# Performance work log

Measured on AMD Instinct MI355X. Metric: run time of the kernel, lower is better.

Reference implementation:

```python
import jax, jax.numpy as jnp
import numpy as np

N, M, D, O = 1_000_000, 64, 3, 2


def _rbf(A, B, sf, ell):
    # squared-exponential kernel: sf^2 * exp(-||a/ell - b/ell||^2 / 2)
    A = A / ell
    B = B / ell
    sq = (jnp.sum(A * A, axis=1)[:, None]
          + jnp.sum(B * B, axis=1)[None, :]
          - 2.0 * (A @ B.T))
    return (sf * sf) * jnp.exp(-sq / 2.0)


def setup_inputs() -> dict:
    key = jax.random.key(0)
    k1, k2, k3, k4 = jax.random.split(key, 4)
    X = jax.random.uniform(k1, (N, D), dtype=jnp.float32) * 10.0  # query points
    t = jax.random.normal(k2, (N,), dtype=jnp.float32)            # unused by forward (matches torch)
    Z = jax.random.uniform(k3, (M, D), dtype=jnp.float32) * 10.0  # inducing points (well-separated -> Kzz well-conditioned)
    U = jax.random.normal(k4, (M, O), dtype=jnp.float32)          # learned inducing outputs
    return {"t": t, "X": X, "Z": Z, "U": U, "sf": 1.0, "ell": 1.0}


def reference(t, X, Z, U, sf, ell):
    # Precompute (as in __init__): Kzz, its inverse, Cholesky factor, and their product.
    Kzz = _rbf(Z, Z, sf, ell)                      # [M, M]
    L = jnp.linalg.cholesky(Kzz)                   # [M, M]
    KzzinvL = jnp.linalg.inv(Kzz) @ L              # [M, M]
    # Forward: T = K(X, Z) @ KzzinvL ; out = T @ U
    Kxz = _rbf(X, Z, sf, ell)                      # [N, M] -- dominant memory traffic
    return (Kxz @ KzzinvL) @ U                     # [N, O]
```

## Files before the change

kernel.cpp:

```cpp
#include <hip/hip_runtime.h>
#include <hip/hip_bf16.h>
#include <utility>

#define LOG2E 1.4426950408889634f

#if __has_builtin(__builtin_amdgcn_exp2f)
#define EXP2F(x) __builtin_amdgcn_exp2f(x)
#else
#define EXP2F(x) exp2f(x)
#endif

#if __has_builtin(__builtin_amdgcn_rsqf)
#define RSQ(x) __builtin_amdgcn_rsqf(x)
#else
#define RSQ(x) (1.0f / sqrtf(x))
#endif

#define RDLANE(x, l) __int_as_float(__builtin_amdgcn_readlane(__float_as_int(x), (l)))

typedef float f16v __attribute__((ext_vector_type(16)));
struct Rows { f16v v0, v1, v2, v3; };

template<int J> __device__ __forceinline__ float getR(const Rows& r) {
    if constexpr (J < 16)      return r.v0[J];
    else if constexpr (J < 32) return r.v1[J - 16];
    else if constexpr (J < 48) return r.v2[J - 32];
    else                       return r.v3[J - 48];
}
template<int J> __device__ __forceinline__ void setR(Rows& r, float x) {
    if constexpr (J < 16)      r.v0[J] = x;
    else if constexpr (J < 32) r.v1[J - 16] = x;
    else if constexpr (J < 48) r.v2[J - 32] = x;
    else                       r.v3[J - 48] = x;
}

template<int LO, int W>
__device__ __forceinline__ float selR(const Rows& r, int k) {
    if constexpr (W == 1) {
        return getR<LO>(r);
    } else {
        float lo = selR<LO, W / 2>(r, k);
        float hi = selR<LO + W / 2, W / 2>(r, k);
        return (k & (W / 2)) ? hi : lo;
    }
}

template<int Q>
__device__ __forceinline__ void upd_quad(Rows& r, float lk, const float4 lv) {
    setR<4 * Q + 0>(r, fmaf(-lk, lv.x, getR<4 * Q + 0>(r)));
    setR<4 * Q + 1>(r, fmaf(-lk, lv.y, getR<4 * Q + 1>(r)));
    setR<4 * Q + 2>(r, fmaf(-lk, lv.z, getR<4 * Q + 2>(r)));
    setR<4 * Q + 3>(r, fmaf(-lk, lv.w, getR<4 * Q + 3>(r)));
}
template<int QLO, int... Qs>
__device__ __forceinline__ void upd_quads(Rows& r, float lk, const float4* lkb4,
                                          std::integer_sequence<int, Qs...>) {
    (upd_quad<QLO + Qs>(r, lk, lkb4[QLO + Qs]), ...);
}

template<int... Js>
__device__ __forceinline__ void load_row(Rows& r, const float* Lrow,
                                         std::integer_sequence<int, Js...>) {
    (setR<Js>(r, Lrow[Js]), ...);
}

template<int KLO, int KHI, int ULO>
__device__ __forceinline__ void chol_phase(Rows& r, float* Lsh, float* lkbuf,
                                           int lane) {
    const float4* lkb4 = (const float4*)lkbuf;
#pragma clang loop unroll(disable)
    for (int k = KLO; k < KHI; ++k) {
        float rk  = selR<ULO, 64 - ULO>(r, k);
        float dk  = RDLANE(rk, k);
        float inv = RSQ(dk);
        float lk  = rk * inv;
        float st  = (lane == k) ? inv : lk;
        Lsh[lane * 65 + k] = st;
        lkbuf[lane] = lk;
        __syncthreads();
        upd_quads<ULO / 4>(r, lk, lkb4,
                           std::make_integer_sequence<int, 16 - ULO / 4>{});
        __syncthreads();
    }
}

__global__ __launch_bounds__(64, 1)
void gp_precompute(const float* __restrict__ Z, const float* __restrict__ U,
                   const float* __restrict__ sf_p, const float* __restrict__ ell_p,
                   float* __restrict__ ws) {
    __shared__ float Lsh[64 * 65];
    __shared__ float4 zbuf[64];
    __shared__ __align__(16) float lkbuf[64];
    const int lane = threadIdx.x;
    const float sf  = sf_p[0];
    const float ell = ell_p[0];
    const float inv_ell = 1.0f / ell;
    const float sf2 = sf * sf;

    const float z0 = Z[lane * 3 + 0] * inv_ell;
    const float z1 = Z[lane * 3 + 1] * inv_ell;
    const float z2 = Z[lane * 3 + 2] * inv_ell;

    zbuf[lane] = make_float4(z0, z1, z2, 0.0f);
    __syncthreads();

#pragma unroll 4
    for (int j = 0; j < 64; ++j) {
        float4 zj = zbuf[j];
        float dx = z0 - zj.x;
        float dy = z1 - zj.y;
        float dz = z2 - zj.z;
        float sq = dx * dx + dy * dy + dz * dz;
        Lsh[lane * 65 + j] = sf2 * EXP2F(-0.5f * LOG2E * sq);
    }
    __syncthreads();

    Rows r;
    load_row(r, &Lsh[lane * 65], std::make_integer_sequence<int, 64>{});

    chol_phase< 0, 32,  0>(r, Lsh, lkbuf, lane);
    chol_phase<32, 48, 32>(r, Lsh, lkbuf, lane);
    chol_phase<48, 64, 48>(r, Lsh, lkbuf, lane);
    __syncthreads();

    float s0 = U[lane * 2 + 0];
    float s1 = U[lane * 2 + 1];
    float w0v = 0.0f, w1v = 0.0f;
#pragma unroll 8
    for (int i = 63; i >= 0; --i) {
        float a   = Lsh[i * 65 + lane];
        float rdi = RDLANE(a, i);
        float w0  = RDLANE(s0, i) * rdi;
        float w1  = RDLANE(s1, i) * rdi;
        bool  me  = (lane == i);
        w0v = me ? w0 : w0v;
        w1v = me ? w1 : w1v;
        s0 = fmaf(-a, w0, s0);
        s1 = fmaf(-a, w1, s1);
    }

    const float dm = -0.5f * LOG2E * (z0 * z0 + z1 * z1 + z2 * z2);
    float4* ws4 = (float4*)ws;
    ws4[lane * 2 + 0] = make_float4(z0, z1, z2, dm);
    ws4[lane * 2 + 1] = make_float4(sf2 * w0v, sf2 * w1v, 0.0f, 0.0f);
}

__global__ __launch_bounds__(256) void gp_forward(const float* __restrict__ X,
                                                  const float* __restrict__ ws,
                                                  const float* __restrict__ ell_p,
                                                  float* __restrict__ out, int n) {
    __shared__ float4 P[128];
    for (int i = threadIdx.x; i < 128; i += 256)
        P[i] = ((const float4*)ws)[i];
    const float inv_ell = 1.0f / ell_p[0];
    __syncthreads();

    const int t  = blockIdx.x * 256 + threadIdx.x;
    const int i0 = 2 * t;

    float p00, p01, p02, p10, p11, p12;
    if (i0 + 1 < n) {
        const float2* X2 = (const float2*)X;
        float2 xa = X2[3 * t + 0];
        float2 xb = X2[3 * t + 1];
        float2 xc = X2[3 * t + 2];
        p00 = xa.x; p01 = xa.y; p02 = xb.x;
        p10 = xb.y; p11 = xc.x; p12 = xc.y;
    } else if (i0 < n) {
        p00 = X[3 * i0 + 0]; p01 = X[3 * i0 + 1]; p02 = X[3 * i0 + 2];
        p10 = p00; p11 = p01; p12 = p02;
    } else {
        p00 = p01 = p02 = p10 = p11 = p12 = 0.0f;
    }

    float xt0[2], xt1[2], xt2[2], c[2];
    {
        float xs0 = p00 * inv_ell, xs1 = p01 * inv_ell, xs2 = p02 * inv_ell;
        c[0]  = -0.5f * LOG2E * (xs0 * xs0 + xs1 * xs1 + xs2 * xs2);
        xt0[0] = xs0 * LOG2E; xt1[0] = xs1 * LOG2E; xt2[0] = xs2 * LOG2E;
        xs0 = p10 * inv_ell; xs1 = p11 * inv_ell; xs2 = p12 * inv_ell;
        c[1]  = -0.5f * LOG2E * (xs0 * xs0 + xs1 * xs1 + xs2 * xs2);
        xt0[1] = xs0 * LOG2E; xt1[1] = xs1 * LOG2E; xt2[1] = xs2 * LOG2E;
    }

    float acc0[2] = {0.f, 0.f};
    float acc1[2] = {0.f, 0.f};

#pragma unroll 4
    for (int m = 0; m < 64; ++m) {
        const float4 a = P[2 * m + 0];
        const float4 b = P[2 * m + 1];
#pragma unroll
        for (int p = 0; p < 2; ++p) {
            float arg = fmaf(xt0[p], a.x,
                        fmaf(xt1[p], a.y,
                        fmaf(xt2[p], a.z, c[p] + a.w)));
            float e = EXP2F(arg);
            acc0[p] = fmaf(e, b.x, acc0[p]);
            acc1[p] = fmaf(e, b.y, acc1[p]);
        }
    }

    if (i0 + 1 < n) {
        ((float4*)out)[t] = make_float4(acc0[0], acc1[0], acc0[1], acc1[1]);
    } else if (i0 < n) {
        ((float2*)out)[i0] = make_float2(acc0[0], acc1[0]);
    }
}

extern "C" void kernel_launch(void* const* d_in, const int* in_sizes, int n_in,
                              void* d_out, int out_size, void* d_ws, size_t ws_size,
                              hipStream_t stream) {
    const float* X    = (const float*)d_in[1];
    const float* Z    = (const float*)d_in[2];
    const float* U    = (const float*)d_in[3];
    const float* sf   = (const float*)d_in[4];
    const float* ell  = (const float*)d_in[5];
    float* out = (float*)d_out;
    float* ws  = (float*)d_ws;
    const int N = in_sizes[1] / 3;

    gp_precompute<<<1, 64, 0, stream>>>(Z, U, sf, ell, ws);

    const int PTS_PER_BLOCK = 256 * 2;
    const int blocks = (N + PTS_PER_BLOCK - 1) / PTS_PER_BLOCK;
    gp_forward<<<blocks, 256, 0, stream>>>(X, ws, ell, out, N);
}
```

Baseline: 38.84 us.

## Fuse Cholesky precompute into forward kernel with per-block redundant factorization

Merges the single-block Cholesky/solve precompute and the per-point forward kernel into one launch. Every block redundantly builds Kzz, factors it and solves for the weights straight into shared memory, then grid-strides over about three point chunks. This removes the second kernel launch, the serialization between the two kernels, and the workspace round trip through global memory. In exchange, every block repeats the serial barrier-heavy factorization with all four waves doing identical work, and the 64-float register row may raise register pressure and lower occupancy in the exp-heavy main loop.

```diff
diff --git a/kernel.cpp b/kernel.cpp
--- a/kernel.cpp
+++ b/kernel.cpp
@@ -84,127 +84,123 @@
     }
 }
 
-__global__ __launch_bounds__(64, 1)
-void gp_precompute(const float* __restrict__ Z, const float* __restrict__ U,
-                   const float* __restrict__ sf_p, const float* __restrict__ ell_p,
-                   float* __restrict__ ws) {
+__global__ __launch_bounds__(256)
+void gp_fused(const float* __restrict__ X, const float* __restrict__ Z,
+              const float* __restrict__ U, const float* __restrict__ sf_p,
+              const float* __restrict__ ell_p, float* __restrict__ out,
+              int n, int nChunks) {
     __shared__ float Lsh[64 * 65];
     __shared__ float4 zbuf[64];
     __shared__ __align__(16) float lkbuf[64];
-    const int lane = threadIdx.x;
+    __shared__ float4 P[128];
+
+    const int lane = threadIdx.x & 63;
     const float sf  = sf_p[0];
     const float ell = ell_p[0];
     const float inv_ell = 1.0f / ell;
     const float sf2 = sf * sf;
 
-    const float z0 = Z[lane * 3 + 0] * inv_ell;
-    const float z1 = Z[lane * 3 + 1] * inv_ell;
-    const float z2 = Z[lane * 3 + 2] * inv_ell;
-
-    zbuf[lane] = make_float4(z0, z1, z2, 0.0f);
-    __syncthreads();
+    {
+        const float z0 = Z[lane * 3 + 0] * inv_ell;
+        const float z1 = Z[lane * 3 + 1] * inv_ell;
+        const float z2 = Z[lane * 3 + 2] * inv_ell;
+
+        zbuf[lane] = make_float4(z0, z1, z2, 0.0f);
+        __syncthreads();
 
 #pragma unroll 4
-    for (int j = 0; j < 64; ++j) {
-        float4 zj = zbuf[j];
-        float dx = z0 - zj.x;
-        float dy = z1 - zj.y;
-        float dz = z2 - zj.z;
-        float sq = dx * dx + dy * dy + dz * dz;
-        Lsh[lane * 65 + j] = sf2 * EXP2F(-0.5f * LOG2E * sq);
-    }
-    __syncthreads();
-
-    Rows r;
-    load_row(r, &Lsh[lane * 65], std::make_integer_sequence<int, 64>{});
-
-    chol_phase< 0, 32,  0>(r, Lsh, lkbuf, lane);
-    chol_phase<32, 48, 32>(r, Lsh, lkbuf, lane);
-    chol_phase<48, 64, 48>(r, Lsh, lkbuf, lane);
-    __syncthreads();
-
-    float s0 = U[lane * 2 + 0];
-    float s1 = U[lane * 2 + 1];
-    float w0v = 0.0f, w1v = 0.0f;
+        for (int j = 0; j < 64; ++j) {
+            float4 zj = zbuf[j];
+            float dx = z0 - zj.x;
+            float dy = z1 - zj.y;
+            float dz = z2 - zj.z;
+            float sq = dx * dx + dy * dy + dz * dz;
+            Lsh[lane * 65 + j] = sf2 * EXP2F(-0.5f * LOG2E * sq);
+        }
+        __syncthreads();
+
+        Rows r;
+        load_row(r, &Lsh[lane * 65], std::make_integer_sequence<int, 64>{});
+
+        chol_phase< 0, 32,  0>(r, Lsh, lkbuf, lane);
+        chol_phase<32, 48, 32>(r, Lsh, lkbuf, lane);
+        chol_phase<48, 64, 48>(r, Lsh, lkbuf, lane);
+        __syncthreads();
+
+        float s0 = U[lane * 2 + 0];
+        float s1 = U[lane * 2 + 1];
+        float w0v = 0.0f, w1v = 0.0f;
 #pragma unroll 8
-    for (int i = 63; i >= 0; --i) {
-        float a   = Lsh[i * 65 + lane];
-        float rdi = RDLANE(a, i);
-        float w0  = RDLANE(s0, i) * rdi;
-        float w1  = RDLANE(s1, i) * rdi;
-        bool  me  = (lane == i);
-        w0v = me ? w0 : w0v;
-        w1v = me ? w1 : w1v;
-        s0 = fmaf(-a, w0, s0);
-        s1 = fmaf(-a, w1, s1);
-    }
-
-    const float dm = -0.5f * LOG2E * (z0 * z0 + z1 * z1 + z2 * z2);
-    float4* ws4 = (float4*)ws;
-    ws4[lane * 2 + 0] = make_float4(z0, z1, z2, dm);
-    ws4[lane * 2 + 1] = make_float4(sf2 * w0v, sf2 * w1v, 0.0f, 0.0f);
-}
-
-__global__ __launch_bounds__(256) void gp_forward(const float* __restrict__ X,
-                                                  const float* __restrict__ ws,
-                                                  const float* __restrict__ ell_p,
-                                                  float* __restrict__ out, int n) {
-    __shared__ float4 P[128];
-    for (int i = threadIdx.x; i < 128; i += 256)
-        P[i] = ((const float4*)ws)[i];
-    const float inv_ell = 1.0f / ell_p[0];
-    __syncthreads();
-
-    const int t  = blockIdx.x * 256 + threadIdx.x;
-    const int i0 = 2 * t;
-
-    float p00, p01, p02, p10, p11, p12;
-    if (i0 + 1 < n) {
-        const float2* X2 = (const float2*)X;
-        float2 xa = X2[3 * t + 0];
-        float2 xb = X2[3 * t + 1];
-        float2 xc = X2[3 * t + 2];
-        p00 = xa.x; p01 = xa.y; p02 = xb.x;
-        p10 = xb.y; p11 = xc.x; p12 = xc.y;
-    } else if (i0 < n) {
-        p00 = X[3 * i0 + 0]; p01 = X[3 * i0 + 1]; p02 = X[3 * i0 + 2];
-        p10 = p00; p11 = p01; p12 = p02;
-    } else {
-        p00 = p01 = p02 = p10 = p11 = p12 = 0.0f;
-    }
-
-    float xt0[2], xt1[2], xt2[2], c[2];
-    {
-        float xs0 = p00 * inv_ell, xs1 = p01 * inv_ell, xs2 = p02 * inv_ell;
-        c[0]  = -0.5f * LOG2E * (xs0 * xs0 + xs1 * xs1 + xs2 * xs2);
-        xt0[0] = xs0 * LOG2E; xt1[0] = xs1 * LOG2E; xt2[0] = xs2 * LOG2E;
-        xs0 = p10 * inv_ell; xs1 = p11 * inv_ell; xs2 = p12 * inv_ell;
-        c[1]  = -0.5f * LOG2E * (xs0 * xs0 + xs1 * xs1 + xs2 * xs2);
-        xt0[1] = xs0 * LOG2E; xt1[1] = xs1 * LOG2E; xt2[1] = xs2 * LOG2E;
-    }
-
-    float acc0[2] = {0.f, 0.f};
-    float acc1[2] = {0.f, 0.f};
+        for (int i = 63; i >= 0; --i) {
+            float a   = Lsh[i * 65 + lane];
+            float rdi = RDLANE(a, i);
+            float w0  = RDLANE(s0, i) * rdi;
+            float w1  = RDLANE(s1, i) * rdi;
+            bool  me  = (lane == i);
+            w0v = me ? w0 : w0v;
+            w1v = me ? w1 : w1v;
+            s0 = fmaf(-a, w0, s0);
+            s1 = fmaf(-a, w1, s1);
+        }
+
+        const float dm = -0.5f * LOG2E * (z0 * z0 + z1 * z1 + z2 * z2);
+        P[2 * lane + 0] = make_float4(z0, z1, z2, dm);
+        P[2 * lane + 1] = make_float4(sf2 * w0v, sf2 * w1v, 0.0f, 0.0f);
+        __syncthreads();
+    }
+
+    for (int chunk = blockIdx.x; chunk < nChunks; chunk += gridDim.x) {
+        const int t  = chunk * 256 + (int)threadIdx.x;
+        const int i0 = 2 * t;
+
+        float p00, p01, p02, p10, p11, p12;
+        if (i0 + 1 < n) {
+            const float2* X2 = (const float2*)X;
+            float2 xa = X2[3 * t + 0];
+            float2 xb = X2[3 * t + 1];
+            float2 xc = X2[3 * t + 2];
+            p00 = xa.x; p01 = xa.y; p02 = xb.x;
+            p10 = xb.y; p11 = xc.x; p12 = xc.y;
+        } else if (i0 < n) {
+            p00 = X[3 * i0 + 0]; p01 = X[3 * i0 + 1]; p02 = X[3 * i0 + 2];
+            p10 = p00; p11 = p01; p12 = p02;
+        } else {
+            p00 = p01 = p02 = p10 = p11 = p12 = 0.0f;
+        }
+
+        float xt0[2], xt1[2], xt2[2], c[2];
+        {
+            float xs0 = p00 * inv_ell, xs1 = p01 * inv_ell, xs2 = p02 * inv_ell;
+            c[0]  = -0.5f * LOG2E * (xs0 * xs0 + xs1 * xs1 + xs2 * xs2);
+            xt0[0] = xs0 * LOG2E; xt1[0] = xs1 * LOG2E; xt2[0] = xs2 * LOG2E;
+            xs0 = p10 * inv_ell; xs1 = p11 * inv_ell; xs2 = p12 * inv_ell;
+            c[1]  = -0.5f * LOG2E * (xs0 * xs0 + xs1 * xs1 + xs2 * xs2);
+            xt0[1] = xs0 * LOG2E; xt1[1] = xs1 * LOG2E; xt2[1] = xs2 * LOG2E;
+        }
+
+        float acc0[2] = {0.f, 0.f};
+        float acc1[2] = {0.f, 0.f};
 
 #pragma unroll 4
-    for (int m = 0; m < 64; ++m) {
-        const float4 a = P[2 * m + 0];
-        const float4 b = P[2 * m + 1];
+        for (int m = 0; m < 64; ++m) {
+            const float4 a = P[2 * m + 0];
+            const float4 b = P[2 * m + 1];
 #pragma unroll
-        for (int p = 0; p < 2; ++p) {
-            float arg = fmaf(xt0[p], a.x,
-                        fmaf(xt1[p], a.y,
-                        fmaf(xt2[p], a.z, c[p] + a.w)));
-            float e = EXP2F(arg);
-            acc0[p] = fmaf(e, b.x, acc0[p]);
-            acc1[p] = fmaf(e, b.y, acc1[p]);
-        }
-    }
-
-    if (i0 + 1 < n) {
-        ((float4*)out)[t] = make_float4(acc0[0], acc1[0], acc0[1], acc1[1]);
-    } else if (i0 < n) {
-        ((float2*)out)[i0] = make_float2(acc0[0], acc1[0]);
+            for (int p = 0; p < 2; ++p) {
+                float arg = fmaf(xt0[p], a.x,
+                            fmaf(xt1[p], a.y,
+                            fmaf(xt2[p], a.z, c[p] + a.w)));
+                float e = EXP2F(arg);
+                acc0[p] = fmaf(e, b.x, acc0[p]);
+                acc1[p] = fmaf(e, b.y, acc1[p]);
+            }
+        }
+
+        if (i0 + 1 < n) {
+            ((float4*)out)[t] = make_float4(acc0[0], acc1[0], acc0[1], acc1[1]);
+        } else if (i0 < n) {
+            ((float2*)out)[i0] = make_float2(acc0[0], acc1[0]);
+        }
     }
 }
 
@@ -217,12 +213,10 @@
     const float* sf   = (const float*)d_in[4];
     const float* ell  = (const float*)d_in[5];
     float* out = (float*)d_out;
-    float* ws  = (float*)d_ws;
     const int N = in_sizes[1] / 3;
 
-    gp_precompute<<<1, 64, 0, stream>>>(Z, U, sf, ell, ws);
-
-    const int PTS_PER_BLOCK = 256 * 2;
-    const int blocks = (N + PTS_PER_BLOCK - 1) / PTS_PER_BLOCK;
-    gp_forward<<<blocks, 256, 0, stream>>>(X, ws, ell, out, N);
-}
+    const int nChunks = (N + 511) / 512;
+    int blocks = (nChunks + 2) / 3;
+    if (blocks < 1) blocks = 1;
+    gp_fused<<<blocks, 256, 0, stream>>>(X, Z, U, sf, ell, out, N, nChunks);
+}
```

Result: slower. 83.00 us (+113.7%).
